# Kernel optimization log

Measured on AMD Instinct MI355X. Metric: run time of the kernel, lower is better.

Reference implementation:

```python
import jax, jax.numpy as jnp
import numpy as np

B, T, E, D = 64, 512, 1024, 1024  # batch, enc timesteps, enc hidden, dec hidden


def setup_inputs() -> dict:
    key = jax.random.key(0)
    ks = jax.random.split(key, 9)
    s = lambda fan_in: 1.0 / np.sqrt(fan_in)
    return {
        "hidden": jax.random.normal(ks[0], (B, D), jnp.float32),
        "decoder_out": jax.random.normal(ks[1], (B, D), jnp.float32),
        "encoder_states": jax.random.normal(ks[2], (T, B, E), jnp.float32),
        # attn: Linear(D+E -> 2E)
        "Wa": jax.random.uniform(ks[3], (2 * E, D + E), jnp.float32, -s(D + E), s(D + E)),
        "ba": jax.random.uniform(ks[4], (2 * E,), jnp.float32, -s(D + E), s(D + E)),
        # attn2: Linear(2E -> 1)
        "w2": jax.random.uniform(ks[5], (1, 2 * E), jnp.float32, -s(2 * E), s(2 * E)),
        "b2": jax.random.uniform(ks[6], (1,), jnp.float32, -s(2 * E), s(2 * E)),
        # attn_combine: Linear(D+E -> D)
        "Wc": jax.random.uniform(ks[7], (D, D + E), jnp.float32, -s(D + E), s(D + E)),
        "bc": jax.random.uniform(ks[8], (D,), jnp.float32, -s(D + E), s(D + E)),
    }


def reference(hidden, decoder_out, encoder_states, Wa, ba, w2, b2, Wc, bc):
    d = hidden.shape[1]
    # attn(cat(hidden, enc_t)) = hidden @ Wa[:, :D].T + enc_t @ Wa[:, D:].T + ba
    h_proj = hidden @ Wa[:, :d].T + ba                      # [B, 2E]
    e_proj = jnp.einsum('tbe,fe->tbf', encoder_states, Wa[:, d:])  # [T, B, 2E]
    act = jnp.tanh(h_proj[None, :, :] + e_proj)             # [T, B, 2E]
    scores = jnp.einsum('tbf,f->bt', act, w2[0]) + b2[0]    # [B, T]
    weights = jax.nn.softmax(scores, axis=-1)               # softmax over timesteps
    # weighted sum of encoder states: [B, E]
    applied = jnp.einsum('bt,tbe->be', weights, encoder_states)
    combined = jnp.concatenate([decoder_out, applied], axis=1)  # [B, D+E]
    out = jnp.tanh(combined @ Wc.T + bc)                    # [B, D]
    return out, applied
```

## Files before the change

### kernel.cpp

```cpp
#include <hip/hip_runtime.h>
#include <hip/hip_bf16.h>

#define BB 64
#define TT 512
#define EE 1024
#define DD 1024

typedef __attribute__((ext_vector_type(8))) short s16x8;
typedef __attribute__((ext_vector_type(4))) float f32x4;

__device__ __forceinline__ float bf2f(unsigned short u) {
    unsigned int x = ((unsigned int)u) << 16;
    return __builtin_bit_cast(float, x);
}
__device__ __forceinline__ unsigned short f2bf(float f) {
    unsigned int u = __builtin_bit_cast(unsigned int, f);
    u += 0x7FFF + ((u >> 16) & 1);
    return (unsigned short)(u >> 16);
}
__device__ __forceinline__ float tanh_fast(float x) {
    x = fminf(fmaxf(x, -15.f), 15.f);
    float e = __expf(2.f * x);
    return (e - 1.f) / (e + 1.f);
}

__global__ __launch_bounds__(256) void conv_enc_kernel(
    const float4* __restrict__ src, ushort4* __restrict__ dst)
{
    int idx = blockIdx.x * 256 + threadIdx.x;
    float4 v = src[idx];
    ushort4 o;
    o.x = f2bf(v.x); o.y = f2bf(v.y); o.z = f2bf(v.z); o.w = f2bf(v.w);
    dst[idx] = o;
}

__global__ __launch_bounds__(256) void conv_wa_kernel(
    const float* __restrict__ Wa, unsigned short* __restrict__ WaR)
{
    int idx = blockIdx.x * 256 + threadIdx.x;
    int row = idx >> 8;
    int c4  = idx & 255;
    float4 v = *(const float4*)(Wa + (size_t)row * 2048 + 1024 + c4 * 4);
    ushort4 o;
    o.x = f2bf(v.x); o.y = f2bf(v.y); o.z = f2bf(v.z); o.w = f2bf(v.w);
    *(ushort4*)(WaR + (size_t)row * 1024 + c4 * 4) = o;
}

__global__ __launch_bounds__(256) void hproj_kernel(
    const float* __restrict__ hidden,
    const float* __restrict__ Wa,
    const float* __restrict__ ba,
    float* __restrict__ hp)
{
    __shared__ float sW[8 * 1024];
    const int tid  = threadIdx.x;
    const int lane = tid & 63;
    const int wave = tid >> 6;
    const int f0   = blockIdx.x * 8;

#pragma unroll
    for (int i = 0; i < 8; ++i) {
        int idx = i * 256 + tid;
        int fi  = idx >> 8;
        int c4  = idx & 255;
        ((float4*)sW)[idx] = *(const float4*)(Wa + (size_t)(f0 + fi) * 2048 + c4 * 4);
    }
    __syncthreads();

    for (int bi = 0; bi < 16; ++bi) {
        int b = wave * 16 + bi;
        float h[16];
#pragma unroll
        for (int j = 0; j < 16; ++j) h[j] = hidden[b * 1024 + lane + 64 * j];
#pragma unroll
        for (int fi = 0; fi < 8; ++fi) {
            float s = 0.f;
#pragma unroll
            for (int j = 0; j < 16; ++j) s += h[j] * sW[fi * 1024 + lane + 64 * j];
#pragma unroll
            for (int m = 32; m; m >>= 1) s += __shfl_xor(s, m);
            if (lane == 0) hp[(f0 + fi) * 64 + b] = s + ba[f0 + fi];
        }
    }
}

__global__ __launch_bounds__(256) void gemm_scores(
    const unsigned short* __restrict__ encB,
    const unsigned short* __restrict__ WaR,
    const float* __restrict__ hp,
    const float* __restrict__ w2,
    float* __restrict__ scores)
{
    __shared__ short sA[128 * 32];
    __shared__ short sB[128 * 32];
    __shared__ float rowAcc[128];

    const int tid  = threadIdx.x;
    const int bm   = blockIdx.x;
    const int bn   = blockIdx.y;
    const int lane = tid & 63;
    const int wave = tid >> 6;
    const int wm   = wave >> 1;
    const int wn   = wave & 1;
    const int c    = lane & 15;
    const int quad = lane >> 4;

    f32x4 acc[4][4];
#pragma unroll
    for (int mi = 0; mi < 4; ++mi)
#pragma unroll
        for (int ni = 0; ni < 4; ++ni)
#pragma unroll
            for (int r = 0; r < 4; ++r) acc[mi][ni][r] = 0.f;

    for (int k0 = 0; k0 < 1024; k0 += 32) {
#pragma unroll
        for (int i = 0; i < 2; ++i) {
            int idx = i * 256 + tid;
            int row = idx >> 2;
            int cg  = idx & 3;
            const unsigned short* ga = encB + (size_t)(bm * 128 + row) * 1024 + k0 + cg * 8;
            __builtin_amdgcn_global_load_lds(
                (const __attribute__((address_space(1))) void*)ga,
                (__attribute__((address_space(3))) void*)&sA[idx * 8], 16, 0, 0);
            const unsigned short* gb = WaR + (size_t)(bn * 128 + row) * 1024 + k0 + cg * 8;
            __builtin_amdgcn_global_load_lds(
                (const __attribute__((address_space(1))) void*)gb,
                (__attribute__((address_space(3))) void*)&sB[idx * 8], 16, 0, 0);
        }
        __builtin_amdgcn_s_waitcnt(0);
        __syncthreads();

        s16x8 aF[4], bF[4];
#pragma unroll
        for (int mi = 0; mi < 4; ++mi)
            aF[mi] = *(const s16x8*)&sA[(wm * 64 + mi * 16 + c) * 32 + quad * 8];
#pragma unroll
        for (int ni = 0; ni < 4; ++ni)
            bF[ni] = *(const s16x8*)&sB[(wn * 64 + ni * 16 + c) * 32 + quad * 8];

#pragma unroll
        for (int mi = 0; mi < 4; ++mi)
#pragma unroll
            for (int ni = 0; ni < 4; ++ni)
                acc[mi][ni] = __builtin_amdgcn_mfma_f32_16x16x32_bf16(
                    aF[mi], bF[ni], acc[mi][ni], 0, 0, 0);

        __syncthreads();
    }

    if (tid < 128) rowAcc[tid] = 0.f;
    __syncthreads();

#pragma unroll
    for (int mi = 0; mi < 4; ++mi) {
#pragma unroll
        for (int r = 0; r < 4; ++r) {
            int lrow = wm * 64 + mi * 16 + quad * 4 + r;
            int grow = bm * 128 + lrow;
            int b    = grow & 63;
            float s = 0.f;
#pragma unroll
            for (int ni = 0; ni < 4; ++ni) {
                int f = bn * 128 + wn * 64 + ni * 16 + c;
                float v = acc[mi][ni][r] + hp[f * 64 + b];
                s += tanh_fast(v) * w2[f];
            }
            s += __shfl_xor(s, 1);
            s += __shfl_xor(s, 2);
            s += __shfl_xor(s, 4);
            s += __shfl_xor(s, 8);
            if (c == 0) atomicAdd(&rowAcc[lrow], s);
        }
    }
    __syncthreads();
    if (tid < 128) {
        int grow = bm * 128 + tid;
        int b = grow & 63;
        int t = grow >> 6;
        atomicAdd(&scores[b * TT + t], rowAcc[tid]);
    }
}

__global__ __launch_bounds__(256) void softmax_kernel(float* __restrict__ scores)
{
    __shared__ float wmax[4];
    __shared__ float wsum[4];
    const int b   = blockIdx.x;
    const int tid = threadIdx.x;
    float* row = scores + b * TT;

    float v0 = row[tid], v1 = row[tid + 256];
    float m = fmaxf(v0, v1);
#pragma unroll
    for (int s = 32; s; s >>= 1) m = fmaxf(m, __shfl_xor(m, s));
    if ((tid & 63) == 0) wmax[tid >> 6] = m;
    __syncthreads();
    m = fmaxf(fmaxf(wmax[0], wmax[1]), fmaxf(wmax[2], wmax[3]));

    float e0 = __expf(v0 - m), e1 = __expf(v1 - m);
    float s = e0 + e1;
#pragma unroll
    for (int t = 32; t; t >>= 1) s += __shfl_xor(s, t);
    if ((tid & 63) == 0) wsum[tid >> 6] = s;
    __syncthreads();
    float inv = 1.f / (wsum[0] + wsum[1] + wsum[2] + wsum[3]);
    row[tid]       = e0 * inv;
    row[tid + 256] = e1 * inv;
}

__global__ __launch_bounds__(256) void applied_part_kernel(
    const unsigned short* __restrict__ encB,
    const float* __restrict__ w,
    float* __restrict__ part)
{
    __shared__ float red[128 * 8];
    const int tc  = blockIdx.x;
    const int b   = blockIdx.y;
    const int tid = threadIdx.x;
    const int eo  = tid & 127;
    const int th  = tid >> 7;
    const int e0  = eo * 8;

    float a[8];
#pragma unroll
    for (int j = 0; j < 8; ++j) a[j] = 0.f;

    for (int it = 0; it < 16; ++it) {
        int t = tc * 32 + th * 16 + it;
        float wt = w[b * TT + t];
        s16x8 v = *(const s16x8*)(encB + ((size_t)(t * BB + b)) * EE + e0);
#pragma unroll
        for (int j = 0; j < 8; ++j) a[j] += wt * bf2f((unsigned short)v[j]);
    }
    if (th == 1) {
#pragma unroll
        for (int j = 0; j < 8; ++j) red[eo * 8 + j] = a[j];
    }
    __syncthreads();
    if (th == 0) {
        float* dst = part + ((size_t)tc * 64 + b) * 1024 + e0;
#pragma unroll
        for (int j = 0; j < 8; ++j) dst[j] = a[j] + red[eo * 8 + j];
    }
}

__global__ __launch_bounds__(256) void applied_reduce_kernel(
    const float* __restrict__ part, float* __restrict__ out_applied)
{
    int idx = blockIdx.x * 256 + threadIdx.x;
    float s = 0.f;
#pragma unroll
    for (int tc = 0; tc < 16; ++tc) s += part[tc * 65536 + idx];
    out_applied[idx] = s;
}

__global__ __launch_bounds__(256) void combine_kernel(
    const float* __restrict__ dec,
    const float* applied,
    const float* __restrict__ Wc,
    const float* __restrict__ bc,
    float* out0)
{
    const int g    = blockIdx.x * 4 + (threadIdx.x >> 6);
    const int lane = threadIdx.x & 63;
    const int d    = g >> 6;
    const int b    = g & 63;

    const float4* wc4 = (const float4*)Wc + (size_t)d * 512;
    const float4* de4 = (const float4*)dec + (size_t)b * 256;
    const float4* ap4 = (const float4*)applied + (size_t)b * 256;

    float s = 0.f;
#pragma unroll
    for (int j = 0; j < 4; ++j) {
        float4 a = de4[j * 64 + lane];
        float4 wv = wc4[j * 64 + lane];
        s += a.x * wv.x + a.y * wv.y + a.z * wv.z + a.w * wv.w;
    }
#pragma unroll
    for (int j = 0; j < 4; ++j) {
        float4 a = ap4[j * 64 + lane];
        float4 wv = wc4[256 + j * 64 + lane];
        s += a.x * wv.x + a.y * wv.y + a.z * wv.z + a.w * wv.w;
    }
#pragma unroll
    for (int m = 32; m; m >>= 1) s += __shfl_xor(s, m);
    if (lane == 0) out0[b * DD + d] = tanh_fast(s + bc[d]);
}

extern "C" void kernel_launch(void* const* d_in, const int* in_sizes, int n_in,
                              void* d_out, int out_size, void* d_ws, size_t ws_size,
                              hipStream_t stream) {
    const float* hidden = (const float*)d_in[0];
    const float* dec    = (const float*)d_in[1];
    const float* enc    = (const float*)d_in[2];
    const float* Wa     = (const float*)d_in[3];
    const float* ba     = (const float*)d_in[4];
    const float* w2     = (const float*)d_in[5];
    const float* Wc     = (const float*)d_in[7];
    const float* bc     = (const float*)d_in[8];
    float* out = (float*)d_out;

    unsigned short* encB = (unsigned short*)d_ws;
    unsigned short* WaR  = encB + (size_t)33554432;
    float* hp     = (float*)(WaR + (size_t)2097152);
    float* scores = hp + 131072;
    float* part   = scores + 32768;

    hipMemsetAsync(scores, 0, BB * TT * sizeof(float), stream);
    conv_enc_kernel<<<32768, 256, 0, stream>>>((const float4*)enc, (ushort4*)encB);
    conv_wa_kernel<<<2048, 256, 0, stream>>>(Wa, WaR);
    hproj_kernel<<<256, 256, 0, stream>>>(hidden, Wa, ba, hp);
    dim3 g2(256, 16);
    gemm_scores<<<g2, 256, 0, stream>>>(encB, WaR, hp, w2, scores);
    softmax_kernel<<<BB, 256, 0, stream>>>(scores);
    dim3 g3(16, 64);
    applied_part_kernel<<<g3, 256, 0, stream>>>(encB, scores, part);
    applied_reduce_kernel<<<256, 256, 0, stream>>>(part, out + BB * DD);
    combine_kernel<<<16384, 256, 0, stream>>>(dec, out + BB * DD, Wc, bc, out);
}
```

Measured before the change: 575.7 us.

## Double K-tile depth and reorder LDS layout for conflict-free MFMA fragment loads

The gemm_scores K-step grows from 32 to 64, halving the number of barrier/load/wait iterations. The LDS tiles are rearranged so each 16-row fragment group is stored contiguously in lane order, making the MFMA fragment reads linear and free of bank conflicts. The epilogue now loads hp as float4 vectors and hoists w2 into registers. Doubled LDS use (32KB per block) may reduce occupancy, and there is still no double buffering.

```diff
diff --git a/kernel.cpp b/kernel.cpp
--- a/kernel.cpp
+++ b/kernel.cpp
@@ -5,6 +5,7 @@
 #define TT 512
 #define EE 1024
 #define DD 1024
+#define BK 64
 
 typedef __attribute__((ext_vector_type(8))) short s16x8;
 typedef __attribute__((ext_vector_type(4))) float f32x4;
@@ -91,8 +92,8 @@
     const float* __restrict__ w2,
     float* __restrict__ scores)
 {
-    __shared__ short sA[128 * 32];
-    __shared__ short sB[128 * 32];
+    __shared__ short sA[128 * BK];
+    __shared__ short sB[128 * BK];
     __shared__ float rowAcc[128];
 
     const int tid  = threadIdx.x;
@@ -113,64 +114,72 @@
 #pragma unroll
             for (int r = 0; r < 4; ++r) acc[mi][ni][r] = 0.f;
 
-    for (int k0 = 0; k0 < 1024; k0 += 32) {
-#pragma unroll
-        for (int i = 0; i < 2; ++i) {
-            int idx = i * 256 + tid;
-            int row = idx >> 2;
-            int cg  = idx & 3;
-            const unsigned short* ga = encB + (size_t)(bm * 128 + row) * 1024 + k0 + cg * 8;
+    for (int k0 = 0; k0 < 1024; k0 += BK) {
+#pragma unroll
+        for (int i = 0; i < 4; ++i) {
+            int s   = i * 256 + tid;
+            int p   = s >> 7;
+            int g   = (s >> 4) & 7;
+            int rr  = s & 15;
+            int row = p * 16 + rr;
+            const unsigned short* ga = encB + (size_t)(bm * 128 + row) * 1024 + k0 + g * 8;
             __builtin_amdgcn_global_load_lds(
                 (const __attribute__((address_space(1))) void*)ga,
-                (__attribute__((address_space(3))) void*)&sA[idx * 8], 16, 0, 0);
-            const unsigned short* gb = WaR + (size_t)(bn * 128 + row) * 1024 + k0 + cg * 8;
+                (__attribute__((address_space(3))) void*)&sA[s * 8], 16, 0, 0);
+            const unsigned short* gb = WaR + (size_t)(bn * 128 + row) * 1024 + k0 + g * 8;
             __builtin_amdgcn_global_load_lds(
                 (const __attribute__((address_space(1))) void*)gb,
-                (__attribute__((address_space(3))) void*)&sB[idx * 8], 16, 0, 0);
+                (__attribute__((address_space(3))) void*)&sB[s * 8], 16, 0, 0);
         }
         __builtin_amdgcn_s_waitcnt(0);
         __syncthreads();
 
-        s16x8 aF[4], bF[4];
-#pragma unroll
-        for (int mi = 0; mi < 4; ++mi)
-            aF[mi] = *(const s16x8*)&sA[(wm * 64 + mi * 16 + c) * 32 + quad * 8];
+#pragma unroll
+        for (int kk = 0; kk < 2; ++kk) {
+            s16x8 aF[4], bF[4];
+#pragma unroll
+            for (int mi = 0; mi < 4; ++mi)
+                aF[mi] = *(const s16x8*)&sA[((wm * 4 + mi) * 128 + kk * 64 + lane) * 8];
+#pragma unroll
+            for (int ni = 0; ni < 4; ++ni)
+                bF[ni] = *(const s16x8*)&sB[((wn * 4 + ni) * 128 + kk * 64 + lane) * 8];
+
+#pragma unroll
+            for (int mi = 0; mi < 4; ++mi)
+#pragma unroll
+                for (int ni = 0; ni < 4; ++ni)
+                    acc[mi][ni] = __builtin_amdgcn_mfma_f32_16x16x32_bf16(
+                        aF[mi], bF[ni], acc[mi][ni], 0, 0, 0);
+        }
+        __syncthreads();
+    }
+
+    float w2v[4];
+#pragma unroll
+    for (int ni = 0; ni < 4; ++ni) w2v[ni] = w2[bn * 128 + wn * 64 + ni * 16 + c];
+
+    if (tid < 128) rowAcc[tid] = 0.f;
+    __syncthreads();
+
+#pragma unroll
+    for (int mi = 0; mi < 4; ++mi) {
+        int lrow0 = wm * 64 + mi * 16 + quad * 4;
+        int b0    = (bm * 128 + lrow0) & 63;
+        f32x4 hp4[4];
 #pragma unroll
         for (int ni = 0; ni < 4; ++ni)
-            bF[ni] = *(const s16x8*)&sB[(wn * 64 + ni * 16 + c) * 32 + quad * 8];
-
-#pragma unroll
-        for (int mi = 0; mi < 4; ++mi)
+            hp4[ni] = *(const f32x4*)&hp[(bn * 128 + wn * 64 + ni * 16 + c) * 64 + b0];
+#pragma unroll
+        for (int r = 0; r < 4; ++r) {
+            float s = 0.f;
 #pragma unroll
             for (int ni = 0; ni < 4; ++ni)
-                acc[mi][ni] = __builtin_amdgcn_mfma_f32_16x16x32_bf16(
-                    aF[mi], bF[ni], acc[mi][ni], 0, 0, 0);
-
-        __syncthreads();
-    }
-
-    if (tid < 128) rowAcc[tid] = 0.f;
-    __syncthreads();
-
-#pragma unroll
-    for (int mi = 0; mi < 4; ++mi) {
-#pragma unroll
-        for (int r = 0; r < 4; ++r) {
-            int lrow = wm * 64 + mi * 16 + quad * 4 + r;
-            int grow = bm * 128 + lrow;
-            int b    = grow & 63;
-            float s = 0.f;
-#pragma unroll
-            for (int ni = 0; ni < 4; ++ni) {
-                int f = bn * 128 + wn * 64 + ni * 16 + c;
-                float v = acc[mi][ni][r] + hp[f * 64 + b];
-                s += tanh_fast(v) * w2[f];
-            }
+                s += tanh_fast(acc[mi][ni][r] + hp4[ni][r]) * w2v[ni];
             s += __shfl_xor(s, 1);
             s += __shfl_xor(s, 2);
             s += __shfl_xor(s, 4);
             s += __shfl_xor(s, 8);
-            if (c == 0) atomicAdd(&rowAcc[lrow], s);
+            if (c == 0) atomicAdd(&rowAcc[lrow0 + r], s);
         }
     }
     __syncthreads();
```

Measured after the change: 608.1 us. 1.06x slower.
